# Kernel tuning notes

Hardware: AMD Instinct MI355X
Metric: run time of the kernel (lower is better)

## Reference

```python
import jax, jax.numpy as jnp
import numpy as np

B, VN, LN = 32, 576, 128
V_DIM, L_DIM, E, H = 1024, 768, 1024, 16
D = E // H
SCALE = H ** -0.5  # note: original scales by num_heads**-0.5, NOT head_dim**-0.5


def _xavier(key, shape):
    fan_in, fan_out = shape[1], shape[0]
    lim = np.sqrt(6.0 / (fan_in + fan_out))
    return jax.random.uniform(key, shape, jnp.float32, -lim, lim)


def setup_inputs() -> dict:
    key = jax.random.key(0)
    ks = jax.random.split(key, 10)
    return {
        "v": jax.random.normal(ks[0], (B, VN, V_DIM), jnp.float32),
        "l": jax.random.normal(ks[1], (B, LN, L_DIM), jnp.float32),
        "attention_mask_l": jnp.zeros((LN,), jnp.float32),
        "Wvq": _xavier(ks[2], (E, V_DIM)), "bvq": jnp.zeros((E,), jnp.float32),
        "Wlk": _xavier(ks[3], (E, L_DIM)), "blk": jnp.zeros((E,), jnp.float32),
        "Wvv": _xavier(ks[4], (E, V_DIM)), "bvv": jnp.zeros((E,), jnp.float32),
        "Wlv": _xavier(ks[5], (E, L_DIM)), "blv": jnp.zeros((E,), jnp.float32),
        "Wvo": _xavier(ks[6], (V_DIM, E)), "bvo": jnp.zeros((V_DIM,), jnp.float32),
        "Wlo": _xavier(ks[7], (L_DIM, E)), "blo": jnp.zeros((L_DIM,), jnp.float32),
    }


def reference(v, l, attention_mask_l, Wvq, bvq, Wlk, blk, Wvv, bvv, Wlv, blv, Wvo, bvo, Wlo, blo):
    # mode='vl'; dropout is identity (eval mode)
    q = (v @ Wvq.T + bvq).reshape(B, VN, H, D)          # vision queries
    k = (l @ Wlk.T + blk).reshape(B, LN, H, D)          # language keys
    vv = (v @ Wvv.T + bvv).reshape(B, VN, H, D)         # vision values
    lv = (l @ Wlv.T + blv).reshape(B, LN, H, D)         # language values

    attn = jnp.einsum('bqhd,bkhd->bhqk', q, k) * SCALE   # [B,H,vN,lN]
    attn_v = attn + attention_mask_l[None, None, None, :]
    attn_v = jax.nn.softmax(attn_v, axis=-1)             # softmax over lN
    attn_l = jax.nn.softmax(attn, axis=-2)               # transposed softmax over vN

    xl = jnp.einsum('bhqk,bqhd->bkhd', attn_l, vv).reshape(B, LN, E)
    xv = jnp.einsum('bhqk,bkhd->bqhd', attn_v, lv).reshape(B, VN, E)

    xl = xl @ Wlo.T + blo
    xv = xv @ Wvo.T + bvo
    return xv, xl
```

## Files before the change

kernel.cpp:

```cpp
#include <hip/hip_runtime.h>
#include <stdint.h>


typedef unsigned short bfu;
typedef __attribute__((ext_vector_type(4))) float f32x4;
typedef __attribute__((ext_vector_type(8))) short short8;
typedef __attribute__((ext_vector_type(4))) unsigned short u16x4;

#define MFMA16(a,b,c) __builtin_amdgcn_mfma_f32_16x16x32_bf16((a),(b),(c),0,0,0)
#define SCALE_QK 0.25f

__device__ __forceinline__ unsigned short f2bf(float x) {
  unsigned int u = __float_as_uint(x);
  u += 0x7fffu + ((u >> 16) & 1u);
  return (unsigned short)(u >> 16);
}

__device__ __forceinline__ void gload_lds16(const void* g, void* l) {
  __builtin_amdgcn_global_load_lds(
      reinterpret_cast<__attribute__((address_space(1))) void*>(
          reinterpret_cast<uintptr_t>(g)),
      reinterpret_cast<__attribute__((address_space(3))) void*>(
          (uint32_t)reinterpret_cast<uintptr_t>(l)),
      16, 0, 0);
}

__global__ void cvt_f32_bf16(const float* __restrict__ x, bfu* __restrict__ y, int n4) {
  for (int i = blockIdx.x * blockDim.x + threadIdx.x; i < n4; i += gridDim.x * blockDim.x) {
    const float4 f = *reinterpret_cast<const float4*>(x + (size_t)i * 4);
    u16x4 o;
    o[0] = f2bf(f.x); o[1] = f2bf(f.y); o[2] = f2bf(f.z); o[3] = f2bf(f.w);
    *reinterpret_cast<u16x4*>(y + (size_t)i * 4) = o;
  }
}

struct CvtArgs {
  const float* src[7];
  bfu* dst[7];
  int n4[7];
};

__global__ void cvt_multi(CvtArgs a) {
  const int s = blockIdx.y;
  const float* __restrict__ x = a.src[s];
  bfu* __restrict__ y = a.dst[s];
  const int n4 = a.n4[s];
  for (int i = blockIdx.x * blockDim.x + threadIdx.x; i < n4; i += gridDim.x * blockDim.x) {
    const float4 f = *reinterpret_cast<const float4*>(x + (size_t)i * 4);
    u16x4 o;
    o[0] = f2bf(f.x); o[1] = f2bf(f.y); o[2] = f2bf(f.z); o[3] = f2bf(f.w);
    *reinterpret_cast<u16x4*>(y + (size_t)i * 4) = o;
  }
}

__global__ void bias_concat(const float* __restrict__ a, const float* __restrict__ b,
                            const float* __restrict__ c2, const float* __restrict__ d,
                            float* __restrict__ qv, float* __restrict__ kl) {
  const int i = threadIdx.x * 4;
  const float4* s;
  float* o;
  switch (blockIdx.x) {
    case 0: s = (const float4*)a;  o = qv;        break;
    case 1: s = (const float4*)b;  o = qv + 1024; break;
    case 2: s = (const float4*)c2; o = kl;        break;
    default: s = (const float4*)d; o = kl + 1024; break;
  }
  *reinterpret_cast<float4*>(o + i) = s[threadIdx.x];
}

__global__ __launch_bounds__(256) void gemm_bt(
    const bfu* __restrict__ A, const bfu* __restrict__ W, const float* __restrict__ bias,
    bfu* __restrict__ Cb, float* __restrict__ Cf, bfu* __restrict__ Ct, int R, int colsplit,
    int ldc, int M, int N, int K, int nbn)
{
  __shared__ bfu As[128 * 32];
  __shared__ bfu Bs[128 * 32];
  const int nbm = M >> 7;
  const int bid = blockIdx.x;
  int bm, bn;
  if ((nbm & 7) == 0) {
    const int xcd = bid & 7, j = bid >> 3;
    const int jm = j / nbn;
    bm = xcd * (nbm >> 3) + jm;
    bn = j - jm * nbn;
  } else { bm = bid / nbn; bn = bid - (bid / nbn) * nbn; }

  const int t = threadIdx.x, l = t & 63, w = t >> 6;
  const int g = l >> 4, c = l & 15;
  const int wr = (w >> 1) * 64, wc = (w & 1) * 64;

  f32x4 zero = {0.f, 0.f, 0.f, 0.f};
  f32x4 acc[4][4];
  for (int m = 0; m < 4; ++m)
    for (int n = 0; n < 4; ++n) acc[m][n] = zero;

  const int rowA = l >> 2;
  const int kb   = (l & 3) * 16;

  for (int k0 = 0; k0 < K; k0 += 32) {
#pragma unroll
    for (int i = 0; i < 2; ++i) {
      int chunk = w * 2 + i;
      int r = chunk * 16 + rowA;
      const char* ga = (const char*)(A + (size_t)(bm * 128 + r) * K + k0) + kb;
      const char* gb = (const char*)(W + (size_t)(bn * 128 + r) * K + k0) + kb;
      gload_lds16(ga, (char*)As + chunk * 1024);
      gload_lds16(gb, (char*)Bs + chunk * 1024);
    }
    __syncthreads();
    short8 a[4], bf[4];
#pragma unroll
    for (int m = 0; m < 4; ++m)
      a[m] = *reinterpret_cast<const short8*>(&As[(wr + m * 16 + c) * 32 + g * 8]);
#pragma unroll
    for (int n = 0; n < 4; ++n)
      bf[n] = *reinterpret_cast<const short8*>(&Bs[(wc + n * 16 + c) * 32 + g * 8]);
#pragma unroll
    for (int m = 0; m < 4; ++m)
#pragma unroll
      for (int n = 0; n < 4; ++n)
        acc[m][n] = MFMA16(a[m], bf[n], acc[m][n]);
    __syncthreads();
  }

#pragma unroll
  for (int n = 0; n < 4; ++n) {
    const int col = bn * 128 + wc + n * 16 + c;
    const float bs = bias[col];
    if (col >= colsplit) {
      const int colp = col - colsplit;
      const int hh = colp >> 6, dd = colp & 63;
#pragma unroll
      for (int m = 0; m < 4; ++m) {
        const int row0 = bm * 128 + wr + m * 16 + g * 4;
        const int bb = row0 / R, q0 = row0 - bb * R;
        u16x4 pk;
#pragma unroll
        for (int r = 0; r < 4; ++r) pk[r] = f2bf(acc[m][n][r] + bs);
        *reinterpret_cast<u16x4*>(Ct + ((size_t)(bb * 16 + hh) * 64 + dd) * R + q0) = pk;
      }
    } else {
#pragma unroll
      for (int m = 0; m < 4; ++m) {
        const int row0 = bm * 128 + wr + m * 16 + g * 4;
#pragma unroll
        for (int r = 0; r < 4; ++r) {
          float val = acc[m][n][r] + bs;
          size_t idx = (size_t)(row0 + r) * ldc + col;
          if (Cf) Cf[idx] = val;
          else    Cb[idx] = f2bf(val);
        }
      }
    }
  }
}

template<int RT>
__global__ __launch_bounds__(512, 2) void gemm288(
    const bfu* __restrict__ A, const bfu* __restrict__ W, const float* __restrict__ bias,
    bfu* __restrict__ Cb, float* __restrict__ Cf, bfu* __restrict__ Ct, int colsplit,
    int ldc, int M, int N, int K, int nbn)
{
  __shared__ bfu lds[2 * 36864];

  const int tid = threadIdx.x;
  const int w = tid >> 6, lane = tid & 63;
  const int g = lane >> 4, c = lane & 15;
  const int wr = w >> 2, wc = w & 3;
  const int rb0 = wr ? 208 : 0;
  const int rb1 = wr ? 144 : 80;

  const int nbm = M / 288;
  int bm, bn;
  { const int xcd = blockIdx.x & 7, j = blockIdx.x >> 3;
    const int jm = j / nbn; bm = xcd * (nbm >> 3) + jm; bn = j - jm * nbn; }

  const int nt = K >> 6;

  const int srow8 = lane >> 3;
  const int sslot = lane & 7;
  const int swzE  = ((sslot * 16) ^ (srow8 << 4)) >> 1;
  const bfu* srcA = A + (size_t)(bm * 288 + 8 * w + srow8) * K + swzE;
  const bfu* srcB = W + (size_t)(bn * 256 + 8 * w + srow8) * K + swzE;

#define AB(cur) (lds + (cur) * 36864)
#define BB(cur) (lds + (cur) * 36864 + 20480)
#define STAGE_A(cur, j, k0) gload_lds16(srcA + (size_t)(64 * (j)) * K + (k0), \
    (void*)(AB(cur) + (64 * (j) + 8 * w) * 64))
#define STAGE_B(cur, j, k0) gload_lds16(srcB + (size_t)(64 * (j)) * K + (k0), \
    (void*)(BB(cur) + (64 * (j) + 8 * w) * 64))

  short8 aF[5][2], bF[4][2];
  const int swzR = ((c & 7) << 3);

#define LDA(cur, mh, CNT) { _Pragma("unroll") for (int mi2 = 0; mi2 < (CNT); ++mi2) \
    _Pragma("unroll") for (int ks = 0; ks < 2; ++ks) \
      aF[mi2][ks] = *reinterpret_cast<const short8*>( \
        AB(cur) + (((mh) ? rb1 : rb0) + mi2 * 16 + c) * 64 + ((ks * 32 + g * 8) ^ swzR)); }
#define LDB(cur, nh) { _Pragma("unroll") for (int ni2 = 0; ni2 < 2; ++ni2) \
    _Pragma("unroll") for (int ks = 0; ks < 2; ++ks) \
      bF[(nh) * 2 + ni2][ks] = *reinterpret_cast<const short8*>( \
        BB(cur) + (wc * 64 + (nh) * 32 + ni2 * 16 + c) * 64 + ((ks * 32 + g * 8) ^ swzR)); }

  f32x4 acc[9][4];
  const f32x4 zero = {0.f, 0.f, 0.f, 0.f};
#pragma unroll
  for (int mi = 0; mi < 9; ++mi)
#pragma unroll
    for (int ni = 0; ni < 4; ++ni) acc[mi][ni] = zero;

#define PH_MFMA(mh, nh, CNT) { __builtin_amdgcn_s_setprio(1); \
    _Pragma("unroll") for (int mi2 = 0; mi2 < (CNT); ++mi2) \
    _Pragma("unroll") for (int ni2 = 0; ni2 < 2; ++ni2) \
    _Pragma("unroll") for (int ks = 0; ks < 2; ++ks) \
      acc[(mh) * 5 + mi2][(nh) * 2 + ni2] = \
        MFMA16(aF[mi2][ks], bF[(nh) * 2 + ni2][ks], acc[(mh) * 5 + mi2][(nh) * 2 + ni2]); \
    __builtin_amdgcn_s_setprio(0); }

  STAGE_B(0, 0, 0); STAGE_B(0, 1, 0); STAGE_B(0, 2, 0); STAGE_B(0, 3, 0);
  STAGE_A(0, 0, 0); STAGE_A(0, 1, 0); STAGE_A(0, 3, 0); STAGE_A(0, 4, 0); STAGE_A(0, 2, 0);
  asm volatile("s_waitcnt vmcnt(0)" ::: "memory");
  __builtin_amdgcn_s_barrier();

  int cur = 0;
  for (int t = 0; t < nt - 1; ++t) {
    const int k1 = (t + 1) * 64;
    LDB(cur, 0); LDA(cur, 0, 5);
    STAGE_B(cur ^ 1, 0, k1); STAGE_B(cur ^ 1, 1, k1);
    STAGE_B(cur ^ 1, 2, k1); STAGE_B(cur ^ 1, 3, k1);
    __builtin_amdgcn_s_barrier();
    PH_MFMA(0, 0, 5);
    __builtin_amdgcn_s_barrier();
    LDB(cur, 1);
    STAGE_A(cur ^ 1, 0, k1); STAGE_A(cur ^ 1, 1, k1);
    STAGE_A(cur ^ 1, 3, k1); STAGE_A(cur ^ 1, 4, k1);
    asm volatile("s_waitcnt vmcnt(8)" ::: "memory");
    __builtin_amdgcn_s_barrier();
    PH_MFMA(0, 1, 5);
    __builtin_amdgcn_s_barrier();
    LDA(cur, 1, 4);
    STAGE_A(cur ^ 1, 2, k1);
    __builtin_amdgcn_s_barrier();
    PH_MFMA(1, 0, 4);
    __builtin_amdgcn_s_barrier();
    asm volatile("s_waitcnt vmcnt(1)" ::: "memory");
    __builtin_amdgcn_s_barrier();
    PH_MFMA(1, 1, 4);
    __builtin_amdgcn_s_barrier();
    cur ^= 1;
  }
  LDB(cur, 0); LDA(cur, 0, 5);
  __builtin_amdgcn_s_barrier();
  PH_MFMA(0, 0, 5);
  __builtin_amdgcn_s_barrier();
  LDB(cur, 1);
  asm volatile("s_waitcnt vmcnt(0)" ::: "memory");
  __builtin_amdgcn_s_barrier();
  PH_MFMA(0, 1, 5);
  __builtin_amdgcn_s_barrier();
  LDA(cur, 1, 4);
  PH_MFMA(1, 0, 4);
  PH_MFMA(1, 1, 4);

  const bool isCt = (RT > 0) && (bn * 256 >= colsplit);

  if (isCt) {
    const int RTl = (RT > 0 ? RT : 1);
    short* bw = (short*)lds + w * 2432;
#pragma unroll
    for (int ni = 0; ni < 4; ++ni) {
      const float bs = bias[bn * 256 + wc * 64 + ni * 16 + c];
#pragma unroll
      for (int mh = 0; mh < 2; ++mh)
#pragma unroll
        for (int mi2 = 0; mi2 < 5; ++mi2) {
          if (mh == 1 && mi2 == 4) continue;
          const int qlb = wr ? (mh ? 0 : 64) : (mh ? 80 : 0);
          u16x4 pk;
#pragma unroll
          for (int r = 0; r < 4; ++r) pk[r] = f2bf(acc[mh * 5 + mi2][ni][r] + bs);
          *reinterpret_cast<u16x4*>(&bw[c * 152 + qlb + mi2 * 16 + g * 4]) = pk;
        }
#pragma unroll
      for (int it = 0; it < 5; ++it) {
        const int idx = it * 64 + lane;
        if (idx < 288) {
          const int dd = idx / 18, q8 = idx - dd * 18;
          short8 vx = *reinterpret_cast<const short8*>(&bw[dd * 152 + q8 * 8]);
          const int colp = bn * 256 + wc * 64 + ni * 16 + dd - colsplit;
          const int hh = colp >> 6, dl = colp & 63;
          const int qg = bm * 288 + wr * 144 + q8 * 8;
          const int bb = qg / RTl, q0 = qg - bb * RTl;
          *reinterpret_cast<short8*>(Ct + ((size_t)(bb * 16 + hh) * 64 + dl) * RTl + q0) = vx;
        }
      }
    }
  } else if (Cf) {
    float* bwf = (float*)lds + w * 1088;
    float bs4[4];
#pragma unroll
    for (int ni = 0; ni < 4; ++ni) bs4[ni] = bias[bn * 256 + wc * 64 + ni * 16 + c];
#pragma unroll
    for (int mh = 0; mh < 2; ++mh)
#pragma unroll
      for (int mi2 = 0; mi2 < 5; ++mi2) {
        if (mh == 1 && mi2 == 4) continue;
#pragma unroll
        for (int ni = 0; ni < 4; ++ni)
#pragma unroll
          for (int r = 0; r < 4; ++r)
            bwf[(g * 4 + r) * 68 + ni * 16 + c] = acc[mh * 5 + mi2][ni][r] + bs4[ni];
#pragma unroll
        for (int p = 0; p < 4; ++p) {
          const int rr = lane >> 2;
          const int ch = p * 4 + (lane & 3);
          f32x4 vx = *reinterpret_cast<const f32x4*>(&bwf[rr * 68 + ch * 4]);
          const int row = bm * 288 + (mh ? rb1 : rb0) + mi2 * 16 + rr;
          *reinterpret_cast<f32x4*>(Cf + (size_t)row * ldc + bn * 256 + wc * 64 + ch * 4) = vx;
        }
      }
  } else {
    short* bw = (short*)lds + w * 1216;
    float bs4[4];
#pragma unroll
    for (int ni = 0; ni < 4; ++ni) bs4[ni] = bias[bn * 256 + wc * 64 + ni * 16 + c];
#pragma unroll
    for (int mh = 0; mh < 2; ++mh)
#pragma unroll
      for (int mi2 = 0; mi2 < 5; ++mi2) {
        if (mh == 1 && mi2 == 4) continue;
#pragma unroll
        for (int ni = 0; ni < 4; ++ni)
#pragma unroll
          for (int r = 0; r < 4; ++r)
            bw[(g * 4 + r) * 72 + ni * 16 + c] = (short)f2bf(acc[mh * 5 + mi2][ni][r] + bs4[ni]);
#pragma unroll
        for (int half = 0; half < 2; ++half) {
          const int rr = (lane >> 3) + half * 8;
          const int cc2 = (lane & 7) * 8;
          short8 vx = *reinterpret_cast<const short8*>(&bw[rr * 72 + cc2]);
          const int grow = bm * 288 + (mh ? rb1 : rb0) + mi2 * 16 + rr;
          *reinterpret_cast<short8*>(Cb + (size_t)grow * ldc + bn * 256 + wc * 64 + cc2) = vx;
        }
      }
  }
#undef AB
#undef BB
#undef STAGE_A
#undef STAGE_B
#undef LDA
#undef LDB
#undef PH_MFMA
}

__device__ __forceinline__ int pvt_off(int q, int kbyte) { return q * 256 + (kbyte ^ ((q & 7) << 4)); }

__global__ __launch_bounds__(256) void attn_bi(
    const bfu* __restrict__ Q, const bfu* __restrict__ Kl,
    const bfu* __restrict__ LVt, const bfu* __restrict__ VVt,
    const float* __restrict__ mask,
    bfu* __restrict__ xv, bfu* __restrict__ xl)
{
  __shared__ short Ks[128 * 64];
  __shared__ short LVs[64 * 128];
  __shared__ short PvT[4][2048];
  __shared__ short PkT[4][128 * 24];
  __shared__ float cpart[4][128];

  const int bh = blockIdx.x;
  const int b = bh >> 4, h = bh & 15;
  const int t = threadIdx.x, l = t & 63, w = t >> 6;
  const int g = l >> 4, c = l & 15;

  const bfu* Qp  = Q   + ((size_t)b * 576 * 1024 + h * 64);
  const bfu* Kp  = Kl  + ((size_t)b * 128 * 1024 + h * 64);
  const bfu* LVp = LVt + (size_t)bh * 64 * 128;
  const bfu* VVp = VVt + (size_t)bh * 64 * 576;
  const f32x4 zero = {0.f, 0.f, 0.f, 0.f};

  {
    const int kr = l >> 3;
    const bfu* sK = Kp + (size_t)(w * 8 + kr) * 1024 + (((l & 7) ^ kr) * 8);
#pragma unroll
    for (int i = 0; i < 4; ++i)
      gload_lds16(sK + (size_t)(i * 32) * 1024, (void*)&Ks[(i * 32 + w * 8) * 64]);
    const int lr = l >> 4;
    const int key = (w * 4 + lr) & 7;
    const bfu* sLV = LVp + (size_t)(w * 4 + lr) * 128 + ((l >> 3) & 1) * 64 + (((l & 7) ^ key) * 8);
#pragma unroll
    for (int i = 0; i < 4; ++i)
      gload_lds16(sLV + (size_t)(i * 16) * 128, (void*)&LVs[(i * 16 + w * 4) * 128]);
  }
  float mk[8];
#pragma unroll
  for (int kt = 0; kt < 8; ++kt) mk[kt] = mask[kt * 16 + c];
  __syncthreads();

  char* myPv = (char*)&PvT[w][0];
  short* myPk = &PkT[w][0];
  float colacc[8] = {0, 0, 0, 0, 0, 0, 0, 0};
  f32x4 xlacc[2][4];
#pragma unroll
  for (int kt2 = 0; kt2 < 2; ++kt2)
#pragma unroll
    for (int dt = 0; dt < 4; ++dt) xlacc[kt2][dt] = zero;

  for (int it = 0; it < 9; ++it) {
    const int qt = it * 4 + w;
    f32x4 sacc[8];
#pragma unroll
    for (int kt = 0; kt < 8; ++kt) sacc[kt] = zero;
    __builtin_amdgcn_s_setprio(1);
#pragma unroll
    for (int kk = 0; kk < 2; ++kk) {
      short8 aq = *reinterpret_cast<const short8*>(Qp + (size_t)(qt * 16 + c) * 1024 + kk * 32 + g * 8);
#pragma unroll
      for (int kt = 0; kt < 8; ++kt) {
        short8 bk = *reinterpret_cast<const short8*>(
            &Ks[(kt * 16 + c) * 64 + (((kk * 4 + g) ^ (c & 7)) * 8)]);
        sacc[kt] = MFMA16(aq, bk, sacc[kt]);
      }
    }
    __builtin_amdgcn_s_setprio(0);

    float rs[4] = {0, 0, 0, 0};
#pragma unroll
    for (int kt = 0; kt < 8; ++kt) {
      float ca = 0.f;
      u16x4 pk;
#pragma unroll
      for (int r = 0; r < 4; ++r) {
        float Ev = __expf(fmaf(sacc[kt][r], SCALE_QK, mk[kt]));
        rs[r] += Ev;
        ca += Ev;
        pk[r] = f2bf(Ev);
        *reinterpret_cast<unsigned short*>(myPv + pvt_off(g * 4 + r, 2 * (kt * 16 + c))) = pk[r];
      }
      colacc[kt] += ca;
      *reinterpret_cast<u16x4*>(&myPk[(kt * 16 + c) * 24 + g * 4]) = pk;
    }
#pragma unroll
    for (int r = 0; r < 4; ++r) {
      rs[r] += __shfl_xor(rs[r], 1);
      rs[r] += __shfl_xor(rs[r], 2);
      rs[r] += __shfl_xor(rs[r], 4);
      rs[r] += __shfl_xor(rs[r], 8);
    }

    short8 av[4];
#pragma unroll
    for (int kc = 0; kc < 4; ++kc)
      av[kc] = *reinterpret_cast<const short8*>(myPv + pvt_off(c, kc * 64 + g * 16));
    f32x4 oxv[4];
#pragma unroll
    for (int dt = 0; dt < 4; ++dt) oxv[dt] = zero;
    __builtin_amdgcn_s_setprio(1);
#pragma unroll
    for (int dt = 0; dt < 4; ++dt)
#pragma unroll
      for (int kc = 0; kc < 4; ++kc) {
        short8 bv = *reinterpret_cast<const short8*>(
            &LVs[(dt * 16 + c) * 128 + (kc >> 1) * 64 + ((((kc & 1) * 4 + g) ^ (c & 7)) * 8)]);
        oxv[dt] = MFMA16(av[kc], bv, oxv[dt]);
      }
    __builtin_amdgcn_s_setprio(0);
#pragma unroll
    for (int r = 0; r < 4; ++r) rs[r] = 1.0f / rs[r];

    {
      short* bw = (short*)&PvT[w][0];
#pragma unroll
      for (int dt = 0; dt < 4; ++dt)
#pragma unroll
        for (int r = 0; r < 4; ++r)
          bw[(g * 4 + r) * 72 + dt * 16 + c] = (short)f2bf(oxv[dt][r] * rs[r]);
#pragma unroll
      for (int half = 0; half < 2; ++half) {
        const int rr = (l >> 3) + half * 8;
        const int cc = (l & 7) * 8;
        short8 vx = *reinterpret_cast<const short8*>(&bw[rr * 72 + cc]);
        *reinterpret_cast<short8*>(xv + (size_t)(b * 576 + qt * 16 + rr) * 1024 + h * 64 + cc) = vx;
      }
    }

    __syncthreads();

#pragma unroll
    for (int kt2 = 0; kt2 < 2; ++kt2) {
      const int krow = w * 32 + kt2 * 16 + c;
      short8 ap[2];
#pragma unroll
      for (int ks = 0; ks < 2; ++ks) {
        const int wq = ks * 2 + (g >> 1);
        ap[ks] = *reinterpret_cast<const short8*>(&PkT[wq][krow * 24 + (g & 1) * 8]);
      }
      __builtin_amdgcn_s_setprio(1);
#pragma unroll
      for (int dt = 0; dt < 4; ++dt) {
#pragma unroll
        for (int ks = 0; ks < 2; ++ks) {
          short8 bv = *reinterpret_cast<const short8*>(
              VVp + (size_t)(dt * 16 + c) * 576 + it * 64 + ks * 32 + g * 8);
          xlacc[kt2][dt] = MFMA16(ap[ks], bv, xlacc[kt2][dt]);
        }
      }
      __builtin_amdgcn_s_setprio(0);
    }
    __syncthreads();
  }

#pragma unroll
  for (int kt = 0; kt < 8; ++kt) {
    colacc[kt] += __shfl_xor(colacc[kt], 16);
    colacc[kt] += __shfl_xor(colacc[kt], 32);
  }
  if (g == 0) {
#pragma unroll
    for (int kt = 0; kt < 8; ++kt) cpart[w][kt * 16 + c] = colacc[kt];
  }
  __syncthreads();

  short* bw = (short*)&PvT[w][0];
#pragma unroll
  for (int kt2 = 0; kt2 < 2; ++kt2) {
    float ci[4];
#pragma unroll
    for (int r = 0; r < 4; ++r) {
      const int k = w * 32 + kt2 * 16 + g * 4 + r;
      ci[r] = 1.0f / (cpart[0][k] + cpart[1][k] + cpart[2][k] + cpart[3][k]);
    }
#pragma unroll
    for (int dt = 0; dt < 4; ++dt)
#pragma unroll
      for (int r = 0; r < 4; ++r)
        bw[(g * 4 + r) * 72 + dt * 16 + c] = (short)f2bf(xlacc[kt2][dt][r] * ci[r]);
#pragma unroll
    for (int half = 0; half < 2; ++half) {
      const int rr = (l >> 3) + half * 8;
      const int cc = (l & 7) * 8;
      short8 vx = *reinterpret_cast<const short8*>(&bw[rr * 72 + cc]);
      *reinterpret_cast<short8*>(xl + (size_t)(b * 128 + w * 32 + kt2 * 16 + rr) * 1024 + h * 64 + cc) = vx;
    }
  }
}

static inline int cvt_grid(int n4) {
  int g = (n4 + 255) / 256;
  return g > 4096 ? 4096 : g;
}

extern "C" void kernel_launch(void* const* d_in, const int* in_sizes, int n_in,
                              void* d_out, int out_size, void* d_ws, size_t ws_size,
                              hipStream_t stream)
{
  const float* v    = (const float*)d_in[0];
  const float* lx   = (const float*)d_in[1];
  const float* mask = (const float*)d_in[2];
  const float* Wvq  = (const float*)d_in[3];
  const float* bvq  = (const float*)d_in[4];
  const float* Wlk  = (const float*)d_in[5];
  const float* blk  = (const float*)d_in[6];
  const float* Wvv  = (const float*)d_in[7];
  const float* bvv  = (const float*)d_in[8];
  const float* Wlv  = (const float*)d_in[9];
  const float* blv  = (const float*)d_in[10];
  const float* Wvo  = (const float*)d_in[11];
  const float* bvo  = (const float*)d_in[12];
  const float* Wlo  = (const float*)d_in[13];
  const float* blo  = (const float*)d_in[14];

  float* out_xv = (float*)d_out;
  float* out_xl = out_xv + (size_t)18432 * 1024;

  bfu* ws   = (bfu*)d_ws;
  bfu* vb   = ws;
  bfu* lb   = vb   + 18874368;
  bfu* wqv  = lb   + 3145728;
  bfu* wklv = wqv  + 2097152;
  bfu* wvo  = wklv + 1572864;
  bfu* wlo  = wvo  + 1048576;
  bfu* Qb   = wlo  + 786432;
  bfu* VVt  = Qb   + 18874368;
  bfu* Kb   = VVt  + 18874368;
  bfu* LVt  = Kb   + 4194304;
  float* biasqv = (float*)(LVt + 4194304);
  float* biaskl = biasqv + 2048;

  cvt_f32_bf16<<<cvt_grid(18874368 / 4), 256, 0, stream>>>(v, vb, 18874368 / 4);
  CvtArgs ca;
  ca.src[0] = lx;  ca.dst[0] = lb;             ca.n4[0] = 3145728 / 4;
  ca.src[1] = Wvq; ca.dst[1] = wqv;            ca.n4[1] = 1048576 / 4;
  ca.src[2] = Wvv; ca.dst[2] = wqv + 1048576;  ca.n4[2] = 1048576 / 4;
  ca.src[3] = Wlk; ca.dst[3] = wklv;           ca.n4[3] = 786432 / 4;
  ca.src[4] = Wlv; ca.dst[4] = wklv + 786432;  ca.n4[4] = 786432 / 4;
  ca.src[5] = Wvo; ca.dst[5] = wvo;            ca.n4[5] = 1048576 / 4;
  ca.src[6] = Wlo; ca.dst[6] = wlo;            ca.n4[6] = 786432 / 4;
  cvt_multi<<<dim3(1024, 7), 256, 0, stream>>>(ca);
  bias_concat<<<4, 256, 0, stream>>>(bvq, bvv, blk, blv, biasqv, biaskl);

  gemm288<576><<<64 * 8, 512, 0, stream>>>(vb, wqv, biasqv, Qb, nullptr, VVt, 1024, 1024,
                                           18432, 2048, 1024, 8);
  gemm_bt<<<32 * 16, 256, 0, stream>>>(lb, wklv, biaskl, Kb, nullptr, LVt, 128, 1024, 1024,
                                       4096, 2048, 768, 16);

  attn_bi<<<512, 256, 0, stream>>>(Qb, Kb, LVt, VVt, mask, vb, Kb);

  gemm288<0><<<64 * 4, 512, 0, stream>>>(vb, wvo, bvo, nullptr, out_xv, nullptr, 1 << 30, 1024,
                                         18432, 1024, 1024, 4);
  gemm_bt<<<32 * 6, 256, 0, stream>>>(Kb, wlo, blo, nullptr, out_xl, nullptr, 0, 768, 768,
                                      4096, 768, 1024, 6);
}
```

Baseline: 255.8 us.

## Load GEMM B operand directly from global into registers, skipping LDS staging

The 288x256 projection GEMM no longer stages the weight (B) tile through shared memory. Each wave now loads its MFMA B fragments straight from global memory into registers at the end of every k-step, and only the A tile stays double-buffered in LDS. This cuts LDS footprint and LDS read and write traffic, and removes several barriers and waitcnt phases. In exchange, global B reads are repeated across the two wave rows and are less coalesced, and the next tile's B load latency is exposed right before its first MFMA.

```diff
diff --git a/kernel.cpp b/kernel.cpp
--- a/kernel.cpp
+++ b/kernel.cpp
@@ -161,7 +161,7 @@
     bfu* __restrict__ Cb, float* __restrict__ Cf, bfu* __restrict__ Ct, int colsplit,
     int ldc, int M, int N, int K, int nbn)
 {
-  __shared__ bfu lds[2 * 36864];
+  __shared__ bfu lds[2 * 20480];
 
   const int tid = threadIdx.x;
   const int w = tid >> 6, lane = tid & 63;
@@ -181,26 +181,24 @@
   const int sslot = lane & 7;
   const int swzE  = ((sslot * 16) ^ (srow8 << 4)) >> 1;
   const bfu* srcA = A + (size_t)(bm * 288 + 8 * w + srow8) * K + swzE;
-  const bfu* srcB = W + (size_t)(bn * 256 + 8 * w + srow8) * K + swzE;
-
-#define AB(cur) (lds + (cur) * 36864)
-#define BB(cur) (lds + (cur) * 36864 + 20480)
+
+#define AB(cur) (lds + (cur) * 20480)
 #define STAGE_A(cur, j, k0) gload_lds16(srcA + (size_t)(64 * (j)) * K + (k0), \
     (void*)(AB(cur) + (64 * (j) + 8 * w) * 64))
-#define STAGE_B(cur, j, k0) gload_lds16(srcB + (size_t)(64 * (j)) * K + (k0), \
-    (void*)(BB(cur) + (64 * (j) + 8 * w) * 64))
-
-  short8 aF[5][2], bF[4][2];
+
+  const bfu* srcBd = W + (size_t)(bn * 256 + wc * 64 + c) * K + g * 8;
+  short8 bD[4][2];
+#define LOADB(k0) { _Pragma("unroll") for (int ni = 0; ni < 4; ++ni) \
+    _Pragma("unroll") for (int ks = 0; ks < 2; ++ks) \
+      bD[ni][ks] = *reinterpret_cast<const short8*>(srcBd + (size_t)(ni * 16) * K + (k0) + ks * 32); }
+
+  short8 aF[5][2];
   const int swzR = ((c & 7) << 3);
 
 #define LDA(cur, mh, CNT) { _Pragma("unroll") for (int mi2 = 0; mi2 < (CNT); ++mi2) \
     _Pragma("unroll") for (int ks = 0; ks < 2; ++ks) \
       aF[mi2][ks] = *reinterpret_cast<const short8*>( \
         AB(cur) + (((mh) ? rb1 : rb0) + mi2 * 16 + c) * 64 + ((ks * 32 + g * 8) ^ swzR)); }
-#define LDB(cur, nh) { _Pragma("unroll") for (int ni2 = 0; ni2 < 2; ++ni2) \
-    _Pragma("unroll") for (int ks = 0; ks < 2; ++ks) \
-      bF[(nh) * 2 + ni2][ks] = *reinterpret_cast<const short8*>( \
-        BB(cur) + (wc * 64 + (nh) * 32 + ni2 * 16 + c) * 64 + ((ks * 32 + g * 8) ^ swzR)); }
 
   f32x4 acc[9][4];
   const f32x4 zero = {0.f, 0.f, 0.f, 0.f};
@@ -214,47 +212,38 @@
     _Pragma("unroll") for (int ni2 = 0; ni2 < 2; ++ni2) \
     _Pragma("unroll") for (int ks = 0; ks < 2; ++ks) \
       acc[(mh) * 5 + mi2][(nh) * 2 + ni2] = \
-        MFMA16(aF[mi2][ks], bF[(nh) * 2 + ni2][ks], acc[(mh) * 5 + mi2][(nh) * 2 + ni2]); \
+        MFMA16(aF[mi2][ks], bD[(nh) * 2 + ni2][ks], acc[(mh) * 5 + mi2][(nh) * 2 + ni2]); \
     __builtin_amdgcn_s_setprio(0); }
 
-  STAGE_B(0, 0, 0); STAGE_B(0, 1, 0); STAGE_B(0, 2, 0); STAGE_B(0, 3, 0);
-  STAGE_A(0, 0, 0); STAGE_A(0, 1, 0); STAGE_A(0, 3, 0); STAGE_A(0, 4, 0); STAGE_A(0, 2, 0);
-  asm volatile("s_waitcnt vmcnt(0)" ::: "memory");
+  STAGE_A(0, 0, 0); STAGE_A(0, 1, 0); STAGE_A(0, 2, 0); STAGE_A(0, 3, 0); STAGE_A(0, 4, 0);
+  LOADB(0);
+  asm volatile("s_waitcnt vmcnt(8)" ::: "memory");
   __builtin_amdgcn_s_barrier();
 
   int cur = 0;
   for (int t = 0; t < nt - 1; ++t) {
     const int k1 = (t + 1) * 64;
-    LDB(cur, 0); LDA(cur, 0, 5);
-    STAGE_B(cur ^ 1, 0, k1); STAGE_B(cur ^ 1, 1, k1);
-    STAGE_B(cur ^ 1, 2, k1); STAGE_B(cur ^ 1, 3, k1);
+    LDA(cur, 0, 5);
+    STAGE_A(cur ^ 1, 0, k1); STAGE_A(cur ^ 1, 1, k1);
+    STAGE_A(cur ^ 1, 2, k1); STAGE_A(cur ^ 1, 3, k1); STAGE_A(cur ^ 1, 4, k1);
     __builtin_amdgcn_s_barrier();
     PH_MFMA(0, 0, 5);
-    __builtin_amdgcn_s_barrier();
-    LDB(cur, 1);
-    STAGE_A(cur ^ 1, 0, k1); STAGE_A(cur ^ 1, 1, k1);
-    STAGE_A(cur ^ 1, 3, k1); STAGE_A(cur ^ 1, 4, k1);
-    asm volatile("s_waitcnt vmcnt(8)" ::: "memory");
     __builtin_amdgcn_s_barrier();
     PH_MFMA(0, 1, 5);
     __builtin_amdgcn_s_barrier();
     LDA(cur, 1, 4);
-    STAGE_A(cur ^ 1, 2, k1);
     __builtin_amdgcn_s_barrier();
     PH_MFMA(1, 0, 4);
     __builtin_amdgcn_s_barrier();
-    asm volatile("s_waitcnt vmcnt(1)" ::: "memory");
-    __builtin_amdgcn_s_barrier();
     PH_MFMA(1, 1, 4);
+    LOADB(k1);
+    asm volatile("s_waitcnt vmcnt(8)" ::: "memory");
     __builtin_amdgcn_s_barrier();
     cur ^= 1;
   }
-  LDB(cur, 0); LDA(cur, 0, 5);
+  LDA(cur, 0, 5);
   __builtin_amdgcn_s_barrier();
   PH_MFMA(0, 0, 5);
-  __builtin_amdgcn_s_barrier();
-  LDB(cur, 1);
-  asm volatile("s_waitcnt vmcnt(0)" ::: "memory");
   __builtin_amdgcn_s_barrier();
   PH_MFMA(0, 1, 5);
   __builtin_amdgcn_s_barrier();
@@ -345,11 +334,9 @@
       }
   }
 #undef AB
-#undef BB
 #undef STAGE_A
-#undef STAGE_B
+#undef LOADB
 #undef LDA
-#undef LDB
 #undef PH_MFMA
 }
 
```

Result: slower. 319.6 us (+25.0%).
